# Optimization experiments

Hardware: AMD Instinct MI355X
Metric: run time of the kernel (lower is better)

## Reference

```python
import jax, jax.numpy as jnp
import numpy as np

B, N, D0 = 128, 128, 512   # batch, n_objects, obj_dim
H, KD, R = 32, 64, 16      # n_heads, key_dim, n_relations
D = D0 + 1                 # with temporal tag

def setup_inputs() -> dict:
    key = jax.random.key(0)
    k1, k2, k3, k4, k5 = jax.random.split(key, 5)
    s = 0.02
    return {
        'obj_seq': jax.random.normal(k1, (B, N, D0), jnp.float32),
        'W_k':  jax.random.normal(k2, (KD, D), jnp.float32) * s,
        'W_q1': jax.random.normal(k3, (H * KD, D * N), jnp.float32) * s,
        'W_q2': jax.random.normal(k4, (H * KD, D * N), jnp.float32) * s,
        'W_s':  jax.random.normal(k5, (R, D), jnp.float32) * s,
    }

def reference(obj_seq, W_k, W_q1, W_q2, W_s):
    b, n, _ = obj_seq.shape
    # append temporal tag channel: obj -> [B, N, D]
    tag = jnp.broadcast_to(jnp.arange(n, dtype=obj_seq.dtype)[None, :, None], (b, n, 1))
    obj = jnp.concatenate([obj_seq, tag], axis=2)
    flat = obj.reshape(b, -1)                      # [B, N*D]
    Q1 = (flat @ W_q1.T).reshape(b, H, KD)         # [B, H, KD]
    Q2 = (flat @ W_q2.T).reshape(b, H, KD)
    K = obj @ W_k.T                                # [B, N, KD]
    # scores [B, N, H], softmax over objects (dim=1 in torch)
    A1 = jax.nn.softmax(jnp.einsum('bhk,bnk->bnh', Q1, K), axis=1)
    A2 = jax.nn.softmax(jnp.einsum('bhk,bnk->bnh', Q2, K), axis=1)
    # attention-weighted object sums: [B, H, D]
    E1 = jnp.einsum('bnh,bnd->bhd', A1, obj)
    E2 = jnp.einsum('bnh,bnd->bhd', A2, obj)
    Dr = E1 @ W_s.T - E2 @ W_s.T                   # [B, H, R]
    Dr = jnp.concatenate([Dr, E1[:, :, -1:], E2[:, :, -1:]], axis=2)  # [B, H, R+2]
    return Dr.reshape(b, -1)                       # [B, H*(R+2)]
```

## Files before the change

### kernel.cpp

```cpp
#include <hip/hip_runtime.h>
#include <cstdint>

typedef _Float16 f16;
typedef _Float16 f16x8 __attribute__((ext_vector_type(8)));
typedef float f32x4 __attribute__((ext_vector_type(4)));
typedef float floatx4 __attribute__((ext_vector_type(4)));

#define KTOT 65664
#define KSTEPS 2052
#define DP 544

__device__ __forceinline__ void gload_lds16(const void* g, void* l) {
  __builtin_amdgcn_global_load_lds(
      (const __attribute__((address_space(1))) void*)g,
      (__attribute__((address_space(3))) void*)l, 16, 0, 0);
}

__global__ void prep_flat(const float* __restrict__ obj_seq, f16* __restrict__ flatHL) {
  int base = blockIdx.x * 1024 + threadIdx.x;
#pragma unroll
  for (int j = 0; j < 4; ++j) {
    int o = base + j * 256;
    int kb = o >> 12;
    int rem = o & 4095;
    int bb = rem >> 5;
    int kk = rem & 31;
    int k = kb * 32 + kk;
    int n = k / 513;
    int d = k - n * 513;
    float v = (d < 512) ? obj_seq[(((size_t)(bb << 7) + n) << 9) + d] : (float)n;
    f16 h = (f16)v;
    flatHL[(size_t)kb * 8192 + rem] = h;
    flatHL[(size_t)kb * 8192 + 4096 + rem] = (f16)(v - (float)h);
  }
}

__global__ void prep_obj(const float* __restrict__ obj_seq, f16* __restrict__ objHi,
                         f16* __restrict__ objLo, f16* __restrict__ objT16) {
  __shared__ f16 tile[32][132];
  int b = blockIdx.x / 17, c = blockIdx.x - 17 * (blockIdx.x / 17);
  int t = threadIdx.x;
  if (c < 16) {
#pragma unroll
    for (int i = 0; i < 16; ++i) {
      int e = t + i * 256;
      int n = e >> 5, dd = e & 31;
      float v = obj_seq[(((size_t)(b << 7) + n) << 9) + (c << 5) + dd];
      f16 h = (f16)v;
      objHi[((size_t)((b << 7) + n)) * DP + (c << 5) + dd] = h;
      objLo[((size_t)((b << 7) + n)) * DP + (c << 5) + dd] = (f16)(v - (float)h);
      tile[dd][n] = h;
    }
    __syncthreads();
#pragma unroll
    for (int i = 0; i < 16; ++i) {
      int e = t + i * 256;
      int dd = e >> 7, n = e & 127;
      objT16[(((size_t)b * DP + (c << 5) + dd) << 7) + n] = tile[dd][n];
    }
  } else {
#pragma unroll
    for (int i = 0; i < 16; ++i) {
      int e = t + i * 256;
      int n = e >> 5, dd = e & 31;
      f16 h = (dd == 0) ? (f16)(float)n : (f16)0.f;
      objHi[((size_t)((b << 7) + n)) * DP + 512 + dd] = h;
      objLo[((size_t)((b << 7) + n)) * DP + 512 + dd] = (f16)0.f;
    }
#pragma unroll
    for (int i = 0; i < 16; ++i) {
      int e = t + i * 256;
      int dd = e >> 7, n = e & 127;
      objT16[(((size_t)b * DP + 512 + dd) << 7) + n] = (dd == 0) ? (f16)(float)n : (f16)0.f;
    }
  }
}

__global__ void prep_wk(const float* __restrict__ W_k, f16* __restrict__ WkHi,
                        f16* __restrict__ WkLo) {
  int o = blockIdx.x * 256 + threadIdx.x;
  int kd = o / DP, d = o - kd * DP;
  float v = (d < 513) ? W_k[kd * 513 + d] * 1024.f : 0.f;
  f16 h = (f16)v;
  WkHi[o] = h;
  WkLo[o] = (f16)(v - (float)h);
}

__global__ __launch_bounds__(512, 2) void qgemm(const f16* __restrict__ flatHL,
                                                const float* __restrict__ Wq1,
                                                const float* __restrict__ Wq2,
                                                float* __restrict__ Q) {
  __shared__ f16 As[2][8192];
  const int tid = threadIdx.x;
  const int lane = tid & 63;
  const int wave = tid >> 6;
  const int wm = wave >> 2, wn = wave & 3;
  const int l15 = lane & 15, lk = lane >> 4;
  const int ntile = blockIdx.x & 31;
  const int ksp = blockIdx.x >> 5;
  const int t0 = ksp * 129;
  const int nt = min(129, KSTEPS - t0);
  const float* Wsrc = (ntile < 16) ? (Wq1 + (size_t)ntile * 128 * KTOT)
                                   : (Wq2 + (size_t)(ntile - 16) * 128 * KTOT);
  const float* wrow0 = Wsrc + (size_t)(wn * 32 + l15) * KTOT + (size_t)t0 * 32 + lk * 8;
  const float* wrow1 = wrow0 + (size_t)16 * KTOT;
  const int abyte = (wm * 64 + l15) * 64 + lk * 16;
  const f16* sbase = flatHL + (size_t)t0 * 8192 + tid * 8;

  f32x4 acc[4][2];
#pragma unroll
  for (int mi = 0; mi < 4; ++mi)
#pragma unroll
    for (int nf = 0; nf < 2; ++nf) acc[mi][nf] = (f32x4){0.f, 0.f, 0.f, 0.f};

  gload_lds16(sbase, &As[0][tid * 8]);
  gload_lds16(sbase + 4096, &As[0][4096 + tid * 8]);
  __syncthreads();

  for (int t = 0; t < nt; ++t) {
    const int cur = t & 1;
    floatx4 w0a = *(const floatx4*)(wrow0 + (size_t)t * 32);
    floatx4 w0b = *(const floatx4*)(wrow0 + (size_t)t * 32 + 4);
    floatx4 w1a = *(const floatx4*)(wrow1 + (size_t)t * 32);
    floatx4 w1b = *(const floatx4*)(wrow1 + (size_t)t * 32 + 4);
    if (t + 1 < nt) {
      gload_lds16(sbase + (size_t)(t + 1) * 8192, &As[cur ^ 1][tid * 8]);
      gload_lds16(sbase + (size_t)(t + 1) * 8192 + 4096, &As[cur ^ 1][4096 + tid * 8]);
    }

    f16x8 whi[2], wlo[2];
#pragma unroll
    for (int j = 0; j < 4; ++j) {
      { float v = w0a[j] * 1024.f; f16 h = (f16)v; whi[0][j] = h; wlo[0][j] = (f16)(v - (float)h); }
      { float v = w0b[j] * 1024.f; f16 h = (f16)v; whi[0][4 + j] = h; wlo[0][4 + j] = (f16)(v - (float)h); }
      { float v = w1a[j] * 1024.f; f16 h = (f16)v; whi[1][j] = h; wlo[1][j] = (f16)(v - (float)h); }
      { float v = w1b[j] * 1024.f; f16 h = (f16)v; whi[1][4 + j] = h; wlo[1][4 + j] = (f16)(v - (float)h); }
    }

    f16x8 afh[4], afl[4];
#pragma unroll
    for (int mi = 0; mi < 4; ++mi) {
      afh[mi] = *(const f16x8*)((const char*)&As[cur][0] + abyte + mi * 1024);
      afl[mi] = *(const f16x8*)((const char*)&As[cur][0] + 8192 + abyte + mi * 1024);
    }

#pragma unroll
    for (int mi = 0; mi < 4; ++mi) {
#pragma unroll
      for (int nf = 0; nf < 2; ++nf) {
        acc[mi][nf] = __builtin_amdgcn_mfma_f32_16x16x32_f16(afh[mi], whi[nf], acc[mi][nf], 0, 0, 0);
        acc[mi][nf] = __builtin_amdgcn_mfma_f32_16x16x32_f16(afh[mi], wlo[nf], acc[mi][nf], 0, 0, 0);
        acc[mi][nf] = __builtin_amdgcn_mfma_f32_16x16x32_f16(afl[mi], whi[nf], acc[mi][nf], 0, 0, 0);
      }
    }
    __syncthreads();
  }

  const float s = 1.f / 1024.f;
#pragma unroll
  for (int mi = 0; mi < 4; ++mi) {
    int row = wm * 64 + mi * 16 + lk * 4;
#pragma unroll
    for (int nf = 0; nf < 2; ++nf) {
      int col = ntile * 128 + wn * 32 + nf * 16 + l15;
#pragma unroll
      for (int j = 0; j < 4; ++j) atomicAdd(&Q[(size_t)(row + j) * 4096 + col], acc[mi][nf][j] * s);
    }
  }
}

__global__ __launch_bounds__(512, 1) void predinet_tail(
    const f16* __restrict__ objHi, const f16* __restrict__ objLo, const f16* __restrict__ objT16,
    const f16* __restrict__ WkHi, const f16* __restrict__ WkLo,
    const float* __restrict__ Q, const float* __restrict__ W_s, float* __restrict__ out) {
  __shared__ __align__(16) char smem[105984];
  const int b = blockIdx.x;
  const int tid = threadIdx.x, lane = tid & 63, wave = tid >> 6;
  const int l15 = lane & 15, lk = lane >> 4;

  f16* WT = (f16*)(smem);
  f16* Qh = (f16*)(smem + 17408);
  f16* Ql = (f16*)(smem + 26624);
  f16* Kh = (f16*)(smem + 35840);
  f16* Kl = (f16*)(smem + 54272);
  float* S = (float*)(smem + 72704);
  f16* E = (f16*)(smem + 17408);
  float* DL = (float*)(smem + 96832);

  {
    const float* qsrc = Q + (size_t)b * 4096 + tid * 8;
    floatx4 q0 = *(const floatx4*)qsrc;
    floatx4 q1 = *(const floatx4*)(qsrc + 4);
    int hp = tid >> 3, kd = (tid * 8) & 63;
    f16x8 vh, vl;
#pragma unroll
    for (int j = 0; j < 4; ++j) {
      f16 h0 = (f16)q0[j]; vh[j] = h0; vl[j] = (f16)(q0[j] - (float)h0);
      f16 h1 = (f16)q1[j]; vh[4 + j] = h1; vl[4 + j] = (f16)(q1[j] - (float)h1);
    }
    *(f16x8*)(Qh + hp * 72 + kd) = vh;
    *(f16x8*)(Ql + hp * 72 + kd) = vl;
  }
  {
    f32x4 acc[4];
#pragma unroll
    for (int nf = 0; nf < 4; ++nf) acc[nf] = (f32x4){0.f, 0.f, 0.f, 0.f};
    const f16* arowH = objHi + ((size_t)(b * 128) + wave * 16 + l15) * DP + lk * 8;
    const f16* arowL = objLo + ((size_t)(b * 128) + wave * 16 + l15) * DP + lk * 8;
    const f16* bhi = WkHi + (size_t)l15 * DP + lk * 8;
    const f16* blo = WkLo + (size_t)l15 * DP + lk * 8;
    for (int ks = 0; ks < 17; ++ks) {
      f16x8 ah = *(const f16x8*)(arowH + ks * 32);
      f16x8 al = *(const f16x8*)(arowL + ks * 32);
#pragma unroll
      for (int nf = 0; nf < 4; ++nf) {
        f16x8 h = *(const f16x8*)(bhi + (size_t)nf * 16 * DP + ks * 32);
        f16x8 l = *(const f16x8*)(blo + (size_t)nf * 16 * DP + ks * 32);
        acc[nf] = __builtin_amdgcn_mfma_f32_16x16x32_f16(ah, h, acc[nf], 0, 0, 0);
        acc[nf] = __builtin_amdgcn_mfma_f32_16x16x32_f16(ah, l, acc[nf], 0, 0, 0);
        acc[nf] = __builtin_amdgcn_mfma_f32_16x16x32_f16(al, h, acc[nf], 0, 0, 0);
      }
    }
#pragma unroll
    for (int nf = 0; nf < 4; ++nf)
#pragma unroll
      for (int j = 0; j < 4; ++j) {
        float kv = acc[nf][j] * (1.f / 1024.f);
        f16 h = (f16)kv;
        Kh[(wave * 16 + lk * 4 + j) * 72 + nf * 16 + l15] = h;
        Kl[(wave * 16 + lk * 4 + j) * 72 + nf * 16 + l15] = (f16)(kv - (float)h);
      }
  }
  __syncthreads();
  {
    f32x4 acc[4];
#pragma unroll
    for (int nf = 0; nf < 4; ++nf) acc[nf] = (f32x4){0.f, 0.f, 0.f, 0.f};
#pragma unroll
    for (int ks = 0; ks < 2; ++ks) {
      f16x8 ah = *(const f16x8*)(Kh + (wave * 16 + l15) * 72 + ks * 32 + lk * 8);
      f16x8 al = *(const f16x8*)(Kl + (wave * 16 + l15) * 72 + ks * 32 + lk * 8);
#pragma unroll
      for (int nf = 0; nf < 4; ++nf) {
        f16x8 bh = *(const f16x8*)(Qh + (nf * 16 + l15) * 72 + ks * 32 + lk * 8);
        f16x8 bl = *(const f16x8*)(Ql + (nf * 16 + l15) * 72 + ks * 32 + lk * 8);
        acc[nf] = __builtin_amdgcn_mfma_f32_16x16x32_f16(ah, bh, acc[nf], 0, 0, 0);
        acc[nf] = __builtin_amdgcn_mfma_f32_16x16x32_f16(ah, bl, acc[nf], 0, 0, 0);
        acc[nf] = __builtin_amdgcn_mfma_f32_16x16x32_f16(al, bh, acc[nf], 0, 0, 0);
      }
    }
#pragma unroll
    for (int nf = 0; nf < 4; ++nf)
#pragma unroll
      for (int j = 0; j < 4; ++j)
        S[(wave * 16 + lk * 4 + j) * 65 + nf * 16 + l15] = acc[nf][j];
  }
  __syncthreads();
  {
#pragma unroll
    for (int ci = 0; ci < 8; ++ci) {
      int c = wave * 8 + ci;
      float s0 = S[lane * 65 + c], s1 = S[(lane + 64) * 65 + c];
      float m = fmaxf(s0, s1);
      for (int off = 32; off; off >>= 1) m = fmaxf(m, __shfl_xor(m, off));
      float e0 = __expf(s0 - m), e1 = __expf(s1 - m);
      float sum = e0 + e1;
      for (int off = 32; off; off >>= 1) sum += __shfl_xor(sum, off);
      float inv = 1.f / sum;
      WT[c * 136 + lane] = (f16)(e0 * inv);
      WT[c * 136 + 64 + lane] = (f16)(e1 * inv);
    }
  }
  __syncthreads();
  {
    f16x8 bw[4][4];
#pragma unroll
    for (int nf = 0; nf < 4; ++nf)
#pragma unroll
      for (int ks = 0; ks < 4; ++ks)
        bw[nf][ks] = *(const f16x8*)(WT + (nf * 16 + l15) * 136 + ks * 32 + lk * 8);
    for (int r = 0; r < 5; ++r) {
      int mi = r * 8 + wave;
      if (mi >= 34) break;
      const f16* arow = objT16 + (((size_t)b * DP + mi * 16 + l15) << 7) + lk * 8;
      f16x8 a[4];
#pragma unroll
      for (int ks = 0; ks < 4; ++ks) a[ks] = *(const f16x8*)(arow + ks * 32);
#pragma unroll
      for (int nf = 0; nf < 4; ++nf) {
        f32x4 acc = (f32x4){0.f, 0.f, 0.f, 0.f};
#pragma unroll
        for (int ks = 0; ks < 4; ++ks)
          acc = __builtin_amdgcn_mfma_f32_16x16x32_f16(a[ks], bw[nf][ks], acc, 0, 0, 0);
#pragma unroll
        for (int j = 0; j < 4; ++j)
          E[(mi * 16 + lk * 4 + j) * 73 + nf * 16 + l15] = (f16)acc[j];
      }
    }
  }
  __syncthreads();
  {
    f16* Ws16 = WT;
    for (int i = tid; i < 16 * DP; i += 512) {
      int r = i / DP, d = i - r * DP;
      Ws16[i] = (f16)((d < 513) ? W_s[r * 513 + d] : 0.f);
    }
  }
  __syncthreads();
  if (wave < 4) {
    const f16* Ws16 = WT;
    f32x4 acc = (f32x4){0.f, 0.f, 0.f, 0.f};
    for (int ks = 0; ks < 17; ++ks) {
      f16x8 a = *(const f16x8*)(Ws16 + l15 * DP + ks * 32 + lk * 8);
      f16x8 bv;
#pragma unroll
      for (int jj = 0; jj < 8; ++jj)
        bv[jj] = E[(ks * 32 + lk * 8 + jj) * 73 + wave * 16 + l15];
      acc = __builtin_amdgcn_mfma_f32_16x16x32_f16(a, bv, acc, 0, 0, 0);
    }
#pragma unroll
    for (int j = 0; j < 4; ++j) DL[(lk * 4 + j) * 64 + wave * 16 + l15] = acc[j];
  }
  __syncthreads();
  {
    int h = tid >> 4, r = tid & 15;
    float v = DL[r * 64 + h] - DL[r * 64 + 32 + h];
    out[(size_t)b * 576 + h * 18 + r] = v;
    if (tid < 64) {
      int set = tid >> 5, hh = tid & 31;
      out[(size_t)b * 576 + hh * 18 + 16 + set] = (float)E[512 * 73 + set * 32 + hh];
    }
  }
}

extern "C" void kernel_launch(void* const* d_in, const int* in_sizes, int n_in,
                              void* d_out, int out_size, void* d_ws, size_t ws_size,
                              hipStream_t stream) {
  const float* obj_seq = (const float*)d_in[0];
  const float* W_k = (const float*)d_in[1];
  const float* W_q1 = (const float*)d_in[2];
  const float* W_q2 = (const float*)d_in[3];
  const float* W_s = (const float*)d_in[4];
  float* out = (float*)d_out;

  char* ws = (char*)d_ws;
  size_t off = 0;
  auto carve = [&](size_t bytes) -> char* {
    char* p = ws + off;
    off += (bytes + 255) & ~(size_t)255;
    return p;
  };
  f16* flatHL = (f16*)carve((size_t)KSTEPS * 8192 * 2);
  f16* objHi = (f16*)carve((size_t)16384 * DP * 2);
  f16* objLo = (f16*)carve((size_t)16384 * DP * 2);
  f16* objT16 = (f16*)carve((size_t)128 * DP * 128 * 2);
  f16* WkHi = (f16*)carve((size_t)64 * DP * 2);
  f16* WkLo = (f16*)carve((size_t)64 * DP * 2);
  float* Q = (float*)carve((size_t)128 * 4096 * 4);
  (void)ws_size; (void)in_sizes; (void)n_in; (void)out_size;

  hipMemsetAsync(Q, 0, (size_t)128 * 4096 * 4, stream);
  prep_flat<<<8208, 256, 0, stream>>>(obj_seq, flatHL);
  prep_obj<<<2176, 256, 0, stream>>>(obj_seq, objHi, objLo, objT16);
  prep_wk<<<136, 256, 0, stream>>>(W_k, WkHi, WkLo);
  qgemm<<<512, 512, 0, stream>>>(flatHL, W_q1, W_q2, Q);
  predinet_tail<<<128, 512, 0, stream>>>(objHi, objLo, objT16, WkHi, WkLo, Q, W_s, out);
}
```

Baseline: 432.9 us.

## Stage W_q tiles through LDS with a four-deep async pipeline in qgemm

The Q GEMM now loads both the flat activation tile and the fp32 W_q tile into LDS with direct global-to-LDS loads, using a four-buffer ring with three stages in flight and explicit vmcnt waits. Previously W_q was read straight from global into registers with only double-buffered activations. The activation layout becomes k-major, the W tile uses an XOR swizzle against bank conflicts, and the K-split is halved so the grid is 256 blocks. The aim is to hide the latency of streaming the large weight matrices. The cost is 128 KB of LDS per block, which limits occupancy to one block per CU, plus fewer parallel blocks and longer per-block K loops.

```diff
diff --git a/kernel.cpp b/kernel.cpp
--- a/kernel.cpp
+++ b/kernel.cpp
@@ -16,22 +16,23 @@
       (__attribute__((address_space(3))) void*)l, 16, 0, 0);
 }
 
-__global__ void prep_flat(const float* __restrict__ obj_seq, f16* __restrict__ flatHL) {
+__global__ void prep_flat(const float* __restrict__ obj_seq, f16* __restrict__ flatKM) {
   int base = blockIdx.x * 1024 + threadIdx.x;
 #pragma unroll
   for (int j = 0; j < 4; ++j) {
     int o = base + j * 256;
+    int e = o & 7;
+    int r = (o >> 3) & 127;
+    int k8 = (o >> 10) & 3;
     int kb = o >> 12;
-    int rem = o & 4095;
-    int bb = rem >> 5;
-    int kk = rem & 31;
-    int k = kb * 32 + kk;
+    int k = kb * 32 + k8 * 8 + e;
     int n = k / 513;
     int d = k - n * 513;
-    float v = (d < 512) ? obj_seq[(((size_t)(bb << 7) + n) << 9) + d] : (float)n;
+    float v = (d < 512) ? obj_seq[(((size_t)(r << 7) + n) << 9) + d] : (float)n;
     f16 h = (f16)v;
-    flatHL[(size_t)kb * 8192 + rem] = h;
-    flatHL[(size_t)kb * 8192 + 4096 + rem] = (f16)(v - (float)h);
+    size_t idx = (size_t)kb * 8192 + k8 * 1024 + r * 8 + e;
+    flatKM[idx] = h;
+    flatKM[idx + 4096] = (f16)(v - (float)h);
   }
 }
 
@@ -86,11 +87,11 @@
   WkLo[o] = (f16)(v - (float)h);
 }
 
-__global__ __launch_bounds__(512, 2) void qgemm(const f16* __restrict__ flatHL,
+__global__ __launch_bounds__(512, 2) void qgemm(const f16* __restrict__ flatKM,
                                                 const float* __restrict__ Wq1,
                                                 const float* __restrict__ Wq2,
                                                 float* __restrict__ Q) {
-  __shared__ f16 As[2][8192];
+  __shared__ __align__(16) char smem[131072];
   const int tid = threadIdx.x;
   const int lane = tid & 63;
   const int wave = tid >> 6;
@@ -98,14 +99,30 @@
   const int l15 = lane & 15, lk = lane >> 4;
   const int ntile = blockIdx.x & 31;
   const int ksp = blockIdx.x >> 5;
-  const int t0 = ksp * 129;
-  const int nt = min(129, KSTEPS - t0);
+  const int t0 = ksp * 257;
+  const int nt = min(257, KSTEPS - t0);
   const float* Wsrc = (ntile < 16) ? (Wq1 + (size_t)ntile * 128 * KTOT)
                                    : (Wq2 + (size_t)(ntile - 16) * 128 * KTOT);
-  const float* wrow0 = Wsrc + (size_t)(wn * 32 + l15) * KTOT + (size_t)t0 * 32 + lk * 8;
-  const float* wrow1 = wrow0 + (size_t)16 * KTOT;
-  const int abyte = (wm * 64 + l15) * 64 + lk * 16;
-  const f16* sbase = flatHL + (size_t)t0 * 8192 + tid * 8;
+
+  const int col0 = tid >> 3;
+  const int kh0 = (tid & 7) ^ (col0 & 7);
+  const int col1 = (512 + tid) >> 3;
+  const int kh1 = (tid & 7) ^ (col1 & 7);
+  const float* wsrc0 = Wsrc + (size_t)col0 * KTOT + (size_t)t0 * 32 + kh0 * 4;
+  const float* wsrc1 = Wsrc + (size_t)col1 * KTOT + (size_t)t0 * 32 + kh1 * 4;
+  const f16* asrc = flatKM + (size_t)t0 * 8192 + tid * 8;
+
+  int aoff[4];
+#pragma unroll
+  for (int mi = 0; mi < 4; ++mi) aoff[mi] = lk * 2048 + (wm * 64 + mi * 16 + l15) * 16;
+  int woff[2][2];
+#pragma unroll
+  for (int nf = 0; nf < 2; ++nf) {
+    int col = wn * 32 + nf * 16 + l15;
+    int c7 = col & 7;
+    woff[nf][0] = col * 128 + ((lk * 2) ^ c7) * 16;
+    woff[nf][1] = col * 128 + ((lk * 2 + 1) ^ c7) * 16;
+  }
 
   f32x4 acc[4][2];
 #pragma unroll
@@ -113,36 +130,49 @@
 #pragma unroll
     for (int nf = 0; nf < 2; ++nf) acc[mi][nf] = (f32x4){0.f, 0.f, 0.f, 0.f};
 
-  gload_lds16(sbase, &As[0][tid * 8]);
-  gload_lds16(sbase + 4096, &As[0][4096 + tid * 8]);
-  __syncthreads();
+  auto stage = [&](int tt) {
+    char* As = smem + (tt & 3) * 16384;
+    char* Ws = smem + 65536 + (tt & 3) * 16384;
+    gload_lds16(asrc + (size_t)tt * 8192, As + tid * 16);
+    gload_lds16(asrc + (size_t)tt * 8192 + 4096, As + 8192 + tid * 16);
+    gload_lds16(wsrc0 + (size_t)tt * 32, Ws + tid * 16);
+    gload_lds16(wsrc1 + (size_t)tt * 32, Ws + 8192 + tid * 16);
+  };
+
+  stage(0); stage(1); stage(2);
 
   for (int t = 0; t < nt; ++t) {
-    const int cur = t & 1;
-    floatx4 w0a = *(const floatx4*)(wrow0 + (size_t)t * 32);
-    floatx4 w0b = *(const floatx4*)(wrow0 + (size_t)t * 32 + 4);
-    floatx4 w1a = *(const floatx4*)(wrow1 + (size_t)t * 32);
-    floatx4 w1b = *(const floatx4*)(wrow1 + (size_t)t * 32 + 4);
-    if (t + 1 < nt) {
-      gload_lds16(sbase + (size_t)(t + 1) * 8192, &As[cur ^ 1][tid * 8]);
-      gload_lds16(sbase + (size_t)(t + 1) * 8192 + 4096, &As[cur ^ 1][4096 + tid * 8]);
+    if (t < nt - 2)       asm volatile("s_waitcnt vmcnt(8)" ::: "memory");
+    else if (t == nt - 2) asm volatile("s_waitcnt vmcnt(4)" ::: "memory");
+    else                  asm volatile("s_waitcnt vmcnt(0)" ::: "memory");
+    __builtin_amdgcn_s_barrier();
+    __builtin_amdgcn_sched_barrier(0);
+    if (t + 3 < nt) stage(t + 3);
+
+    const char* As = smem + (t & 3) * 16384;
+    const char* Ws = smem + 65536 + (t & 3) * 16384;
+
+    f16x8 afh[4], afl[4];
+#pragma unroll
+    for (int mi = 0; mi < 4; ++mi) {
+      afh[mi] = *(const f16x8*)(As + aoff[mi]);
+      afl[mi] = *(const f16x8*)(As + 8192 + aoff[mi]);
+    }
+    floatx4 wv[2][2];
+#pragma unroll
+    for (int nf = 0; nf < 2; ++nf) {
+      wv[nf][0] = *(const floatx4*)(Ws + woff[nf][0]);
+      wv[nf][1] = *(const floatx4*)(Ws + woff[nf][1]);
     }
 
     f16x8 whi[2], wlo[2];
 #pragma unroll
-    for (int j = 0; j < 4; ++j) {
-      { float v = w0a[j] * 1024.f; f16 h = (f16)v; whi[0][j] = h; wlo[0][j] = (f16)(v - (float)h); }
-      { float v = w0b[j] * 1024.f; f16 h = (f16)v; whi[0][4 + j] = h; wlo[0][4 + j] = (f16)(v - (float)h); }
-      { float v = w1a[j] * 1024.f; f16 h = (f16)v; whi[1][j] = h; wlo[1][j] = (f16)(v - (float)h); }
-      { float v = w1b[j] * 1024.f; f16 h = (f16)v; whi[1][4 + j] = h; wlo[1][4 + j] = (f16)(v - (float)h); }
-    }
-
-    f16x8 afh[4], afl[4];
-#pragma unroll
-    for (int mi = 0; mi < 4; ++mi) {
-      afh[mi] = *(const f16x8*)((const char*)&As[cur][0] + abyte + mi * 1024);
-      afl[mi] = *(const f16x8*)((const char*)&As[cur][0] + 8192 + abyte + mi * 1024);
-    }
+    for (int nf = 0; nf < 2; ++nf)
+#pragma unroll
+      for (int j = 0; j < 4; ++j) {
+        { float v = wv[nf][0][j] * 1024.f; f16 h = (f16)v; whi[nf][j] = h; wlo[nf][j] = (f16)(v - (float)h); }
+        { float v = wv[nf][1][j] * 1024.f; f16 h = (f16)v; whi[nf][4 + j] = h; wlo[nf][4 + j] = (f16)(v - (float)h); }
+      }
 
 #pragma unroll
     for (int mi = 0; mi < 4; ++mi) {
@@ -153,7 +183,6 @@
         acc[mi][nf] = __builtin_amdgcn_mfma_f32_16x16x32_f16(afl[mi], whi[nf], acc[mi][nf], 0, 0, 0);
       }
     }
-    __syncthreads();
   }
 
   const float s = 1.f / 1024.f;
@@ -350,7 +379,7 @@
     off += (bytes + 255) & ~(size_t)255;
     return p;
   };
-  f16* flatHL = (f16*)carve((size_t)KSTEPS * 8192 * 2);
+  f16* flatKM = (f16*)carve((size_t)KSTEPS * 8192 * 2);
   f16* objHi = (f16*)carve((size_t)16384 * DP * 2);
   f16* objLo = (f16*)carve((size_t)16384 * DP * 2);
   f16* objT16 = (f16*)carve((size_t)128 * DP * 128 * 2);
@@ -360,9 +389,9 @@
   (void)ws_size; (void)in_sizes; (void)n_in; (void)out_size;
 
   hipMemsetAsync(Q, 0, (size_t)128 * 4096 * 4, stream);
-  prep_flat<<<8208, 256, 0, stream>>>(obj_seq, flatHL);
+  prep_flat<<<8208, 256, 0, stream>>>(obj_seq, flatKM);
   prep_obj<<<2176, 256, 0, stream>>>(obj_seq, objHi, objLo, objT16);
   prep_wk<<<136, 256, 0, stream>>>(W_k, WkHi, WkLo);
-  qgemm<<<512, 512, 0, stream>>>(flatHL, W_q1, W_q2, Q);
+  qgemm<<<256, 512, 0, stream>>>(flatKM, W_q1, W_q2, Q);
   predinet_tail<<<128, 512, 0, stream>>>(objHi, objLo, objT16, WkHi, WkLo, Q, W_s, out);
 }
```

Measured after the change: 358.3 us. -17.2%, faster.
